# Kernel tuning notes

Hardware: AMD Instinct MI355X
Metric: run time of the kernel (lower is better)

Reference implementation:

```python
import jax, jax.numpy as jnp
import numpy as np

IN_SHAPE = 640
LEVELS = [3, 4, 5]          # pyramid_levels [3,5] expanded
REG_LEN = 64
NUM_CLASSES = 80
MAX_OUT = 100
SCORE_TH = 0.3
IOU_TH = 0.5
NEG_INF = -1e30


def _make_anchors():
    """Anchor-free anchors: one box per grid cell, grid_zero_start=True,
    anchor_scale=1, aspect_ratio=1 -> half-size = stride/2. Normalized by input size."""
    all_a = []
    for lvl in LEVELS:
        stride = 2 ** lvl
        fs = IN_SHAPE // stride
        hh = np.arange(fs, dtype='float32') * stride
        ww = np.arange(fs, dtype='float32') * stride
        wg, hg = np.meshgrid(ww, hh)
        centers = np.stack([hg, wg], -1).reshape(-1, 2)  # [fs*fs, 2] (h, w)
        half = stride * 0.5
        all_a.append(np.concatenate([centers - half, centers + half], -1))
    return np.concatenate(all_a, 0) / IN_SHAPE  # [8400, 4]


def setup_inputs() -> dict:
    key = jax.random.key(0)
    preds = jax.random.normal(key, (64, 8400, REG_LEN + NUM_CLASSES), dtype=jnp.float32)
    anchors = jnp.asarray(_make_anchors(), dtype=jnp.float32)
    return {"preds": preds, "anchors": anchors}


def _decode_yolov8(preds, anchors):
    bbox_logits, cls_logits = preds[..., :REG_LEN], preds[..., REG_LEN:]
    B, N = bbox_logits.shape[:2]
    bins = REG_LEN // 4  # 16
    d = bbox_logits.reshape(B, N, 4, bins)
    # softmax-weighted DFL expectation over bins
    d = jnp.sum(jax.nn.softmax(d, axis=-1) * jnp.arange(bins, dtype=d.dtype), axis=-1)  # [B,N,4]
    tl, br = d[..., :2], d[..., 2:]
    anchors_hw = anchors[:, 2:] - anchors[:, :2]          # [N,2]
    anchors_ctr = (anchors[:, :2] + anchors[:, 2:]) * 0.5  # [N,2]
    bc = (br - tl) * 0.5 * anchors_hw + anchors_ctr        # center
    bhw = (br + tl) * anchors_hw                           # height/width
    boxes = jnp.concatenate([bc - bhw * 0.5, bc + bhw * 0.5], -1)  # [B,N,4] corners
    return boxes, cls_logits


def _iou_one_vs_all(box, boxes):
    tl = jnp.maximum(box[:2], boxes[:, :2])
    br = jnp.minimum(box[2:], boxes[:, 2:])
    inter = jnp.prod(jnp.clip(br - tl, 0.0, None), -1)
    a1 = jnp.prod(box[2:] - box[:2])
    a2 = jnp.prod(boxes[:, 2:] - boxes[:, :2], -1)
    return inter / (a1 + a2 - inter + 1e-9)


def _nms_single(boxes, scores):
    """Greedy hard NMS for one image. boxes [N,4], scores [N] -> idxs [MAX_OUT] (-1 = invalid)."""
    n = scores.shape[0]
    sc0 = jnp.where(scores > SCORE_TH, scores, NEG_INF)

    def step(sc, _):
        j = jnp.argmax(sc)
        valid = sc[j] > NEG_INF * 0.5
        idx = jnp.where(valid, j, -1).astype(jnp.int32)
        iou = _iou_one_vs_all(boxes[j], boxes)
        sc = jnp.where((iou > IOU_TH) | (jnp.arange(n) == j), NEG_INF, sc)
        return sc, idx

    _, idxs = jax.lax.scan(step, sc0, None, length=MAX_OUT)
    return idxs


def reference(preds, anchors):
    boxes, cls = _decode_yolov8(preds, anchors)       # [B,N,4], [B,N,C]
    scores = jnp.max(cls, -1)                          # [B,N]
    labels = jnp.argmax(cls, -1).astype(jnp.int32)     # [B,N]
    idxs = jax.vmap(_nms_single)(boxes, scores)        # [B,MAX_OUT]
    valid = idxs >= 0
    safe = jnp.maximum(idxs, 0)
    out_boxes = jnp.take_along_axis(boxes, safe[:, :, None], axis=1) * valid[..., None]
    out_scores = jnp.take_along_axis(scores, safe, axis=1) * valid
    out_labels = jnp.where(valid, jnp.take_along_axis(labels, safe, axis=1), -1)
    return out_boxes, out_labels, out_scores
```

## Files before the change

### kernel.cpp

```cpp
#include <hip/hip_runtime.h>

namespace {
constexpr int kB = 64;
constexpr int kN = 8400;
constexpr int kMain = 8192;
constexpr int kTail = kN - kMain;
constexpr int kReg = 64;
constexpr int kCls = 80;
constexpr int kStride = kReg + kCls;
constexpr int kMaxOut = 100;
constexpr float kScoreTh = 0.3f;
constexpr float kIouTh = 0.5f;
}

__global__ __launch_bounds__(256) void decode2_k(
    const float* __restrict__ preds,
    const float* __restrict__ anchors,
    float4* __restrict__ boxes,
    float* __restrict__ scores,
    int* __restrict__ labels,
    unsigned long long* __restrict__ keys)
{
    __shared__ float lds[64 * 148];
    const int tid = threadIdx.x;
    const size_t gbase = (size_t)blockIdx.x * 64;

    const float4* src = (const float4*)(preds + gbase * kStride);
    float4* l4 = (float4*)lds;
#pragma unroll
    for (int k = 0; k < 9; ++k) {
        int i = tid + k * 256;
        int row = i / 36, col = i - row * 36;
        l4[row * 37 + col] = src[i];
    }
    __syncthreads();

    const int a = tid >> 2, s = tid & 3;
    const float* rowp = lds + a * 148;

    float x[16];
    const float4* q = (const float4*)(rowp + s * 16);
#pragma unroll
    for (int j = 0; j < 4; ++j) ((float4*)x)[j] = q[j];
    float m = x[0];
#pragma unroll
    for (int j = 1; j < 16; ++j) m = fmaxf(m, x[j]);
    float se = 0.f, we = 0.f;
#pragma unroll
    for (int j = 0; j < 16; ++j) {
        float t = expf(x[j] - m);
        se += t;
        we += t * (float)j;
    }
    float d = we / se;

    const float4* cl = (const float4*)(rowp + kReg + s * 20);
    float bv = -3e38f; int bi = 0;
#pragma unroll
    for (int c = 0; c < 5; ++c) {
        float4 v = cl[c];
        int cb = s * 20 + 4 * c;
        if (v.x > bv) { bv = v.x; bi = cb; }
        if (v.y > bv) { bv = v.y; bi = cb + 1; }
        if (v.z > bv) { bv = v.z; bi = cb + 2; }
        if (v.w > bv) { bv = v.w; bi = cb + 3; }
    }

    const int lane = tid & 63;
    const int base = lane & ~3;
    float d0 = __shfl(d, base + 0, 64);
    float d1 = __shfl(d, base + 1, 64);
    float d2 = __shfl(d, base + 2, 64);
    float d3 = __shfl(d, base + 3, 64);
    float v1 = __shfl(bv, base + 1, 64); int i1 = __shfl(bi, base + 1, 64);
    float v2 = __shfl(bv, base + 2, 64); int i2 = __shfl(bi, base + 2, 64);
    float v3 = __shfl(bv, base + 3, 64); int i3 = __shfl(bi, base + 3, 64);

    if (s == 0) {
        float best = bv; int bl = bi;
        if (v1 > best) { best = v1; bl = i1; }
        if (v2 > best) { best = v2; bl = i2; }
        if (v3 > best) { best = v3; bl = i3; }

        size_t gi = gbase + a;
        int bimg = (int)(gi / kN);
        int n = (int)(gi - (size_t)bimg * kN);
        float4 av = ((const float4*)anchors)[n];
        float ah0 = av.z - av.x, ah1 = av.w - av.y;
        float c0 = (av.x + av.z) * 0.5f, c1 = (av.y + av.w) * 0.5f;
        float bc0 = (d2 - d0) * 0.5f * ah0 + c0;
        float bc1 = (d3 - d1) * 0.5f * ah1 + c1;
        float bh0 = (d2 + d0) * ah0;
        float bh1 = (d3 + d1) * ah1;
        boxes[gi] = make_float4(bc0 - bh0 * 0.5f, bc1 - bh1 * 0.5f,
                                bc0 + bh0 * 0.5f, bc1 + bh1 * 0.5f);
        scores[gi] = best;
        labels[gi] = bl;

        unsigned long long kkey = ~0ULL;
        if (best > kScoreTh) {
            unsigned u = __float_as_uint(best);
            unsigned o = u ^ ((u & 0x80000000u) ? 0xFFFFFFFFu : 0x80000000u);
            kkey = ((unsigned long long)(~o) << 32) | (unsigned)n;
        }
        keys[((size_t)bimg << 14) + n] = kkey;
    }
}

__global__ __launch_bounds__(512) void sortB_k(unsigned long long* __restrict__ keys)
{
    __shared__ unsigned long long lk[8192];
    unsigned long long* base = keys + ((size_t)blockIdx.x << 14);
    for (int t = threadIdx.x; t < 8192; t += 512) lk[t] = base[t];
    __syncthreads();
    for (int size = 2; size <= 8192; size <<= 1) {
        for (int stride = size >> 1; stride > 0; stride >>= 1) {
#pragma unroll
            for (int p = 0; p < 8; ++p) {
                int n = threadIdx.x + (p << 9);
                int i = ((n & ~(stride - 1)) << 1) | (n & (stride - 1));
                int j = i + stride;
                bool desc = (i & size) != 0;
                unsigned long long a = lk[i], c = lk[j];
                bool sw = desc ? (c > a) : (a > c);
                if (sw) { lk[i] = c; lk[j] = a; }
            }
            __syncthreads();
        }
    }
    for (int t = threadIdx.x; t < 8192; t += 512) base[t] = lk[t];
}

__device__ __forceinline__ unsigned long long getB_(
    const unsigned long long* tailL, int p1, int x)
{
    int t = p1 + x;
    return (t < 256) ? tailL[t] : ~0ULL;
}

__global__ __launch_bounds__(256) void nms_k(
    const float4* __restrict__ boxes,
    const float* __restrict__ scores,
    const int* __restrict__ labels,
    const unsigned long long* __restrict__ keys,
    float* __restrict__ out)
{
    __shared__ unsigned long long tailL[256];
    __shared__ unsigned long long aw[512];
    __shared__ float4 sbox[256];
    __shared__ float  sar[256];
    __shared__ int    sidx[256];
    __shared__ float4 kboxL[kMaxOut];
    __shared__ float  kareaL[kMaxOut];
    __shared__ int    kidxL[kMaxOut];
    __shared__ unsigned long long ballS[4];
    __shared__ int p0S, p1S, kcS, doneS, stopS;

    const int b = blockIdx.x, tid = threadIdx.x;
    const unsigned long long* mainA = keys + ((size_t)b << 14);
    const float4* bx = boxes + (size_t)b * kN;

    if (tid == 0) { p0S = 0; p1S = 0; kcS = 0; doneS = 0; }

    tailL[tid] = (tid < kTail) ? mainA[kMain + tid] : ~0ULL;
    __syncthreads();
    for (int size = 2; size <= 256; size <<= 1) {
        for (int stride = size >> 1; stride > 0; stride >>= 1) {
            if (tid < 128) {
                int i = ((tid & ~(stride - 1)) << 1) | (tid & (stride - 1));
                int j = i + stride;
                bool desc = (i & size) != 0;
                unsigned long long a = tailL[i], c = tailL[j];
                bool sw = desc ? (c > a) : (a > c);
                if (sw) { tailL[i] = c; tailL[j] = a; }
            }
            __syncthreads();
        }
    }

    int kc = 0;
    for (int c = 0; c < 33; ++c) {
        int p0 = p0S, p1 = p1S;
        aw[tid]       = (p0 + tid       < kMain) ? mainA[p0 + tid]       : ~0ULL;
        aw[tid + 256] = (p0 + tid + 256 < kMain) ? mainA[p0 + tid + 256] : ~0ULL;
        __syncthreads();

        int d = tid;
        int lo = 0, hi = d;
        while (lo < hi) {
            int mid = (lo + hi) >> 1;
            bool c2 = getB_(tailL, p1, d - mid - 1) < aw[mid];
            if (c2) hi = mid; else lo = mid + 1;
        }
        unsigned long long av = aw[lo];
        unsigned long long bv = getB_(tailL, p1, d - lo);
        unsigned long long key = (av <= bv) ? av : bv;

        bool alive = (key != ~0ULL);
        int idx = alive ? (int)(key & 0xFFFFFFFFULL) : 0;
        float4 cb = bx[idx];
        float ac = (cb.z - cb.x) * (cb.w - cb.y);

        if (alive) {
            for (int k = 0; k < kc; ++k) {
                float4 kb = kboxL[k];
                float t0 = fmaxf(kb.x, cb.x), t1 = fmaxf(kb.y, cb.y);
                float b0 = fminf(kb.z, cb.z), b1 = fminf(kb.w, cb.w);
                float inter = fmaxf(b0 - t0, 0.f) * fmaxf(b1 - t1, 0.f);
                float iou = inter / (kareaL[k] + ac - inter + 1e-9f);
                if (iou > kIouTh) { alive = false; break; }
            }
        }
        sbox[tid] = cb; sar[tid] = ac; sidx[tid] = idx;
        unsigned long long mm = __ballot((int)alive);
        if ((tid & 63) == 0) ballS[tid >> 6] = mm;
        if (tid == 0) {
            stopS = (key == ~0ULL);
            int lo2 = 0, hi2 = 256;
            while (lo2 < hi2) {
                int mid = (lo2 + hi2) >> 1;
                bool c2 = getB_(tailL, p1, 255 - mid) < aw[mid];
                if (c2) hi2 = mid; else lo2 = mid + 1;
            }
            p0S = p0 + lo2; p1S = p1 + (256 - lo2);
        }
        __syncthreads();
        if (stopS) break;

        if (tid < 64) {
            const int lane = tid;
            unsigned a4 = 0;
#pragma unroll
            for (int j = 0; j < 4; ++j)
                a4 |= (unsigned)((ballS[j] >> lane) & 1ULL) << j;
            int kcl = kc;
            while (true) {
                int jF = -1, lF = 0;
#pragma unroll
                for (int j = 0; j < 4; ++j) {
                    if (jF < 0) {
                        unsigned long long m2 = __ballot((int)((a4 >> j) & 1u));
                        if (m2) { jF = j; lF = __ffsll((unsigned long long)m2) - 1; }
                    }
                }
                if (jF < 0) break;
                int cs = (jF << 6) + lF;
                float4 kb = sbox[cs];
                float kar = sar[cs];
                if (lane == 0) {
                    kboxL[kcl] = kb; kareaL[kcl] = kar; kidxL[kcl] = sidx[cs];
                }
                if (lane == lF) a4 &= ~(1u << jF);
                ++kcl;
                if (kcl == kMaxOut) break;
#pragma unroll
                for (int j = 0; j < 4; ++j) {
                    if ((a4 >> j) & 1u) {
                        float4 cb2 = sbox[lane + (j << 6)];
                        float ac2 = sar[lane + (j << 6)];
                        float t0 = fmaxf(kb.x, cb2.x), t1 = fmaxf(kb.y, cb2.y);
                        float b0 = fminf(kb.z, cb2.z), b1 = fminf(kb.w, cb2.w);
                        float inter = fmaxf(b0 - t0, 0.f) * fmaxf(b1 - t1, 0.f);
                        float iou = inter / (kar + ac2 - inter + 1e-9f);
                        if (iou > kIouTh) a4 &= ~(1u << j);
                    }
                }
            }
            if (lane == 0) { kcS = kcl; if (kcl == kMaxOut) doneS = 1; }
        }
        __syncthreads();
        kc = kcS;
        if (doneS) break;
    }

    int kcf = kcS;
    if (tid < kMaxOut) {
        if (tid < kcf) {
            int idx = kidxL[tid];
            ((float4*)out)[b * kMaxOut + tid] = kboxL[tid];
            out[kB * kMaxOut * 4 + b * kMaxOut + tid] =
                (float)labels[(size_t)b * kN + idx];
            out[kB * kMaxOut * 5 + b * kMaxOut + tid] =
                scores[(size_t)b * kN + idx];
        } else {
            ((float4*)out)[b * kMaxOut + tid] = make_float4(0.f, 0.f, 0.f, 0.f);
            out[kB * kMaxOut * 4 + b * kMaxOut + tid] = -1.0f;
            out[kB * kMaxOut * 5 + b * kMaxOut + tid] = 0.0f;
        }
    }
}

extern "C" void kernel_launch(void* const* d_in, const int* in_sizes, int n_in,
                              void* d_out, int out_size, void* d_ws, size_t ws_size,
                              hipStream_t stream)
{
    const float* preds = (const float*)d_in[0];
    const float* anchors = (const float*)d_in[1];
    float* out = (float*)d_out;

    char* ws = (char*)d_ws;
    float4* boxes = (float4*)ws;
    float* scores = (float*)(ws + (size_t)kB * kN * 16);
    int* labels = (int*)(ws + (size_t)kB * kN * 20);
    unsigned long long* keys =
        (unsigned long long*)(ws + (size_t)kB * kN * 24);

    decode2_k<<<(kB * kN) / 64, 256, 0, stream>>>(preds, anchors, boxes, scores, labels, keys);
    sortB_k<<<kB, 512, 0, stream>>>(keys);
    nms_k<<<kB, 256, 0, stream>>>(boxes, scores, labels, keys, out);
}
```

Baseline: 557.8 us.

## Split per-image bitonic sort into segment sorts plus global merge kernels

After: 512.8 us. 8.1% less time.

```diff
diff --git a/kernel.cpp b/kernel.cpp
--- a/kernel.cpp
+++ b/kernel.cpp
@@ -107,20 +107,23 @@
     }
 }
 
-__global__ __launch_bounds__(512) void sortB_k(unsigned long long* __restrict__ keys)
-{
-    __shared__ unsigned long long lk[8192];
-    unsigned long long* base = keys + ((size_t)blockIdx.x << 14);
-    for (int t = threadIdx.x; t < 8192; t += 512) lk[t] = base[t];
+__global__ __launch_bounds__(512) void sortL_k(unsigned long long* __restrict__ keys)
+{
+    __shared__ unsigned long long lk[2048];
+    const int img = blockIdx.x >> 2, seg = blockIdx.x & 3;
+    const int gofs = seg << 11;
+    unsigned long long* base = keys + ((size_t)img << 14) + gofs;
+
+    for (int t = threadIdx.x; t < 2048; t += 512) lk[t] = base[t];
     __syncthreads();
-    for (int size = 2; size <= 8192; size <<= 1) {
+    for (int size = 2; size <= 2048; size <<= 1) {
         for (int stride = size >> 1; stride > 0; stride >>= 1) {
 #pragma unroll
-            for (int p = 0; p < 8; ++p) {
+            for (int p = 0; p < 2; ++p) {
                 int n = threadIdx.x + (p << 9);
                 int i = ((n & ~(stride - 1)) << 1) | (n & (stride - 1));
                 int j = i + stride;
-                bool desc = (i & size) != 0;
+                bool desc = ((gofs + i) & size) != 0;
                 unsigned long long a = lk[i], c = lk[j];
                 bool sw = desc ? (c > a) : (a > c);
                 if (sw) { lk[i] = c; lk[j] = a; }
@@ -128,7 +131,43 @@
             __syncthreads();
         }
     }
-    for (int t = threadIdx.x; t < 8192; t += 512) base[t] = lk[t];
+    for (int t = threadIdx.x; t < 2048; t += 512) base[t] = lk[t];
+}
+
+__global__ __launch_bounds__(256) void gce_k(unsigned long long* __restrict__ keys)
+{
+    int tg = blockIdx.x * 256 + threadIdx.x;
+    int img = tg >> 12;
+    int n = tg & 4095;
+    unsigned long long* base = keys + ((size_t)img << 14);
+    unsigned long long a = base[n], c = base[n + 4096];
+    if (a > c) { base[n] = c; base[n + 4096] = a; }
+}
+
+template <int SIZE>
+__global__ __launch_bounds__(512) void lm2_k(unsigned long long* __restrict__ keys)
+{
+    __shared__ unsigned long long lk[4096];
+    const int img = blockIdx.x >> 1, half = blockIdx.x & 1;
+    const int gofs = half << 12;
+    unsigned long long* base = keys + ((size_t)img << 14) + gofs;
+
+    for (int t = threadIdx.x; t < 4096; t += 512) lk[t] = base[t];
+    __syncthreads();
+    const bool desc = (gofs & SIZE) != 0;
+    for (int stride = 2048; stride > 0; stride >>= 1) {
+#pragma unroll
+        for (int p = 0; p < 4; ++p) {
+            int n = threadIdx.x + (p << 9);
+            int i = ((n & ~(stride - 1)) << 1) | (n & (stride - 1));
+            int j = i + stride;
+            unsigned long long a = lk[i], c = lk[j];
+            bool sw = desc ? (c > a) : (a > c);
+            if (sw) { lk[i] = c; lk[j] = a; }
+        }
+        __syncthreads();
+    }
+    for (int t = threadIdx.x; t < 4096; t += 512) base[t] = lk[t];
 }
 
 __device__ __forceinline__ unsigned long long getB_(
@@ -306,6 +345,9 @@
         (unsigned long long*)(ws + (size_t)kB * kN * 24);
 
     decode2_k<<<(kB * kN) / 64, 256, 0, stream>>>(preds, anchors, boxes, scores, labels, keys);
-    sortB_k<<<kB, 512, 0, stream>>>(keys);
+    sortL_k<<<kB * 4, 512, 0, stream>>>(keys);
+    lm2_k<4096><<<kB * 2, 512, 0, stream>>>(keys);
+    gce_k<<<(kB * 4096) / 256, 256, 0, stream>>>(keys);
+    lm2_k<8192><<<kB * 2, 512, 0, stream>>>(keys);
     nms_k<<<kB, 256, 0, stream>>>(boxes, scores, labels, keys, out);
 }
```
